# Kernel optimization log

Measured on AMD Instinct MI355X. Metric: run time of the kernel, lower is better.

Reference implementation:

```python
import jax, jax.numpy as jnp
import numpy as np

B = 8388608  # 2^23 rows, ~32MB per [B,1] float32 array
GCD_ITERS = 48  # enough Euclid steps for full int32 range (Fibonacci worst case ~45)


def setup_inputs() -> dict:
    key = jax.random.key(0)
    ka, kb, ko = jax.random.split(key, 3)
    # integer-valued floats in [1, 1e6): avoids division by zero and keeps fp32 exact
    a = jax.random.randint(ka, (B, 1), 1, 1000000).astype(jnp.float32)
    b = jax.random.randint(kb, (B, 1), 1, 1000000).astype(jnp.float32)
    op_type = jax.random.randint(ko, (B, 1), 0, 2).astype(jnp.int32)
    W_mod = jnp.ones((1,), jnp.float32)
    W_gcd = jnp.ones((1,), jnp.float32)
    return {"a": a, "b": b, "op_type": op_type, "W_mod": W_mod, "W_gcd": W_gcd}


def _gcd_int32(x, y):
    # vectorized Euclidean algorithm, fixed iteration count (jit-friendly)
    def body(_, carry):
        x, y = carry
        nz = y != 0
        y_safe = jnp.where(nz, y, 1)
        return (jnp.where(nz, y, x), jnp.where(nz, x % y_safe, 0))
    x, y = jax.lax.fori_loop(0, GCD_ITERS, body, (x, y))
    return x


def reference(a, b, op_type, W_mod, W_gcd):
    # op 0: (a % b) * W_mod ; op 1: gcd(int(a), int(b)) * W_gcd ; else: 0
    mod_out = jnp.mod(a, b) * W_mod
    g = _gcd_int32(a.astype(jnp.int32), b.astype(jnp.int32)).astype(jnp.float32)
    gcd_out = g * W_gcd
    zero = jnp.zeros((), jnp.float32)
    return jnp.where(op_type == 0, mod_out, jnp.where(op_type == 1, gcd_out, zero))
```

## Files before the change

### kernel.cpp

```cpp
#include <hip/hip_runtime.h>


#define TPB 256
#define EPB 1024

__device__ __forceinline__ float euclid_step(float x, float y) {
    float q = floorf(fmaf(x, __builtin_amdgcn_rcpf(y), -0.5f));
    float r = fmaf(-q, y, x);
    return (r >= y) ? r - y : r;
}

extern "C" __global__ void __launch_bounds__(256)
nt_kernel(const float4* __restrict__ a4, const float4* __restrict__ b4,
          const int4* __restrict__ op4, const float* __restrict__ Wm,
          const float* __restrict__ Wg, float4* __restrict__ out4, int n4)
{
    __shared__ __align__(16) float res[EPB];
    __shared__ float qx[EPB];
    __shared__ float qy[EPB];
    __shared__ int   qslot[EPB];
    __shared__ int   cnt;

    const int tid = threadIdx.x;
    if (tid == 0) cnt = 0;
    __syncthreads();

    const float wm = Wm[0];
    const float wg = Wg[0];
    const int i = blockIdx.x * TPB + tid;
    const unsigned lane = tid & 63u;
    const bool valid = (i < n4);

    if (valid) {
        const float4 a = a4[i];
        const float4 b = b4[i];
        const int4  op = op4[i];
        #pragma unroll
        for (int j = 0; j < 4; ++j) {
            const float aj = (&a.x)[j];
            const float bj = (&b.x)[j];
            const int  opj = (&op.x)[j];
            const float r0 = euclid_step(aj, bj);
            res[tid * 4 + j] = (opj == 0) ? r0 * wm : 0.0f;
            const bool need = (opj == 1);
            const unsigned long long mask = __ballot(need);
            const int total = __popcll(mask);
            int base = 0;
            if (lane == 0 && total) base = atomicAdd(&cnt, total);
            base = __shfl(base, 0);
            if (need) {
                const int pos = base + __popcll(mask & ((1ull << lane) - 1ull));
                qx[pos] = bj;
                qy[pos] = r0;
                qslot[pos] = tid * 4 + j;
            }
        }
    }
    __syncthreads();

    const int total = cnt;
    for (int idx = tid; idx < total; idx += TPB) {
        float x = qx[idx];
        float y = qy[idx];
        while (y > 0.0f) {
            const float r = euclid_step(x, y);
            x = y;
            y = r;
        }
        res[qslot[idx]] = x * wg;
    }
    __syncthreads();

    if (valid) {
        out4[i] = ((const float4*)res)[tid];
    }
}

extern "C" void kernel_launch(void* const* d_in, const int* in_sizes, int n_in,
                              void* d_out, int out_size, void* d_ws, size_t ws_size,
                              hipStream_t stream) {
    const float* a   = (const float*)d_in[0];
    const float* b   = (const float*)d_in[1];
    const int*   op  = (const int*)d_in[2];
    const float* Wm  = (const float*)d_in[3];
    const float* Wg  = (const float*)d_in[4];
    float* out = (float*)d_out;

    const int n  = in_sizes[0];
    const int n4 = n >> 2;
    const int blocks = (n4 + TPB - 1) / TPB;

    nt_kernel<<<blocks, TPB, 0, stream>>>(
        (const float4*)a, (const float4*)b, (const int4*)op, Wm, Wg,
        (float4*)out, n4);
}
```

Before: 32.83 us.

## Compact GCD work per wavefront and use least-absolute-remainder Euclid

Replaces the block-wide LDS atomic queue and its two barriers with a per-wavefront compaction. Each wave writes its GCD jobs into its own 256-entry region using ballot prefix counts, then processes them itself, so the block syncs disappear. The Euclid loop now takes min(r, y-r) at each step, which keeps the GCD correct and cuts the iteration count. The cost is worse load balance: a wave with many GCD jobs can no longer share them with other waves in the block.

```diff
diff --git a/kernel.cpp b/kernel.cpp
--- a/kernel.cpp
+++ b/kernel.cpp
@@ -2,9 +2,8 @@
 
 
 #define TPB 256
-#define EPB 1024
 
-__device__ __forceinline__ float euclid_step(float x, float y) {
+__device__ __forceinline__ float mod_step(float x, float y) {
     float q = floorf(fmaf(x, __builtin_amdgcn_rcpf(y), -0.5f));
     float r = fmaf(-q, y, x);
     return (r >= y) ? r - y : r;
@@ -15,22 +14,21 @@
           const int4* __restrict__ op4, const float* __restrict__ Wm,
           const float* __restrict__ Wg, float4* __restrict__ out4, int n4)
 {
-    __shared__ __align__(16) float res[EPB];
-    __shared__ float qx[EPB];
-    __shared__ float qy[EPB];
-    __shared__ int   qslot[EPB];
-    __shared__ int   cnt;
+    __shared__ __align__(16) float res[1024];
+    __shared__ float qb[1024];
+    __shared__ float qr[1024];
+    __shared__ int   qs[1024];
 
-    const int tid = threadIdx.x;
-    if (tid == 0) cnt = 0;
-    __syncthreads();
+    const int tid   = threadIdx.x;
+    const int lane  = tid & 63;
+    const int wbase = (tid >> 6) << 8;
 
+    const int i = blockIdx.x * TPB + tid;
+    const bool valid = (i < n4);
     const float wm = Wm[0];
     const float wg = Wg[0];
-    const int i = blockIdx.x * TPB + tid;
-    const unsigned lane = tid & 63u;
-    const bool valid = (i < n4);
 
+    int qcount = 0;
     if (valid) {
         const float4 a = a4[i];
         const float4 b = b4[i];
@@ -40,36 +38,33 @@
             const float aj = (&a.x)[j];
             const float bj = (&b.x)[j];
             const int  opj = (&op.x)[j];
-            const float r0 = euclid_step(aj, bj);
+            const float r0 = mod_step(aj, bj);
             res[tid * 4 + j] = (opj == 0) ? r0 * wm : 0.0f;
             const bool need = (opj == 1);
             const unsigned long long mask = __ballot(need);
-            const int total = __popcll(mask);
-            int base = 0;
-            if (lane == 0 && total) base = atomicAdd(&cnt, total);
-            base = __shfl(base, 0);
             if (need) {
-                const int pos = base + __popcll(mask & ((1ull << lane) - 1ull));
-                qx[pos] = bj;
-                qy[pos] = r0;
-                qslot[pos] = tid * 4 + j;
+                const int pos = wbase + qcount +
+                    (int)__popcll(mask & ((1ull << lane) - 1ull));
+                qb[pos] = bj;
+                qr[pos] = r0;
+                qs[pos] = tid * 4 + j;
             }
+            qcount += (int)__popcll(mask);
         }
     }
-    __syncthreads();
 
-    const int total = cnt;
-    for (int idx = tid; idx < total; idx += TPB) {
-        float x = qx[idx];
-        float y = qy[idx];
+    for (int k = lane; k < qcount; k += 64) {
+        float x = qb[wbase + k];
+        float y = qr[wbase + k];
+        const int slot = qs[wbase + k];
         while (y > 0.0f) {
-            const float r = euclid_step(x, y);
+            float r = mod_step(x, y);
+            r = fminf(r, y - r);
             x = y;
             y = r;
         }
-        res[qslot[idx]] = x * wg;
+        res[slot] = x * wg;
     }
-    __syncthreads();
 
     if (valid) {
         out4[i] = ((const float4*)res)[tid];
```

Result: faster. 29.59 us (-9.9%).
